# Kernel optimization log

Hardware: AMD Instinct MI355X
Metric: run time of the kernel (lower is better)

## Reference

```python
import math
import jax, jax.numpy as jnp
import numpy as np

B, T, D = 4, 4096, 1024
H = 16            # n_heads
HD = D // H       # head_dim = 64
CAP = int(4096 * 0.125)  # mod capacity k = 512
DFF = int(D * 4 * 2 / 3)  # 2730, per SwiGLU
EPS = 1e-6


def rmsnorm(x, g):
    return x * jax.lax.rsqrt(jnp.mean(x * x, axis=-1, keepdims=True) + EPS) * g


def setup_inputs() -> dict:
    key = jax.random.key(0)
    ks = jax.random.split(key, 9)
    s = lambda k, shape: (jax.random.normal(k, shape, jnp.float32) * 0.02)
    return {
        "x": jax.random.normal(ks[0], (B, T, D), jnp.float32),
        "w_router": s(ks[1], (D,)),          # router Linear(d_model,1,bias=False)
        "W_qkv": s(ks[2], (3 * D, D)),       # torch Linear weight layout [out,in]
        "W_out": s(ks[3], (D, D)),
        "g1": jnp.ones((D,), jnp.float32),   # RMSNorm weights
        "g2": jnp.ones((D,), jnp.float32),
        "W1": s(ks[4], (DFF, D)),
        "W2": s(ks[5], (DFF, D)),
        "W3": s(ks[6], (D, DFF)),
    }


def reference(x, w_router, W_qkv, W_out, g1, g2, W1, W2, W3):
    Bq, Tq, Dq = x.shape
    # --- MoD routing: top-k tokens per sequence (T > capacity) ---
    scores = x @ w_router                         # [B, T]
    _, idx = jax.lax.top_k(scores, CAP)           # [B, k], descending-score order (matches torch.topk)
    x_sel = jnp.take_along_axis(x, idx[:, :, None], axis=1)  # [B, k, D]

    # --- causal attention on the gathered subset ---
    h = rmsnorm(x_sel, g1)
    qkv = (h @ W_qkv.T).reshape(Bq, CAP, 3, H, HD)
    q, k, v = jnp.moveaxis(qkv, 2, 0)             # each [B, k, H, HD]
    att = jnp.einsum('bqhd,bkhd->bhqk', q, k) / math.sqrt(HD)
    mask = jnp.triu(jnp.ones((CAP, CAP), bool), 1)  # causal mask in gathered order
    att = jnp.where(mask, -jnp.inf, att)
    att = jax.nn.softmax(att, axis=-1)
    o = jnp.einsum('bhqk,bkhd->bqhd', att, v).reshape(Bq, CAP, Dq)
    x_attn = o @ W_out.T

    # --- SwiGLU FFN ---
    h2 = rmsnorm(x_sel + x_attn, g2)
    x_ff = (jax.nn.silu(h2 @ W1.T) * (h2 @ W2.T)) @ W3.T

    # --- combine and scatter back into the full sequence ---
    x_proc = x_sel + x_attn + x_ff                # [B, k, D]
    out = x.at[jnp.arange(Bq)[:, None], idx].set(x_proc)
    return out
```

## Files before the change

kernel.cpp:

```cpp
#include <hip/hip_runtime.h>
#include <hip/hip_bf16.h>


#define B_   4
#define T_   4096
#define D_   1024
#define H_   16
#define HD_  64
#define CAP_ 512
#define DFF_ 2730
#define DFFP 2752
#define DFFR 2816
#define M_   (B_*CAP_)

typedef __attribute__((ext_vector_type(8))) short          s16x8;
typedef __attribute__((ext_vector_type(8))) unsigned short u16x8;
typedef __attribute__((ext_vector_type(4))) float          f32x4;

__device__ __forceinline__ float bf2f(unsigned short u) {
    union { float f; unsigned int i; } v; v.i = ((unsigned int)u) << 16; return v.f;
}
__device__ __forceinline__ unsigned short f2bf(float f) {
    union { float f; unsigned int i; } v; v.f = f;
    unsigned int r = v.i + 0x7fffu + ((v.i >> 16) & 1u);
    return (unsigned short)(r >> 16);
}

__device__ __forceinline__ void gload_lds16(const unsigned short* g, unsigned short* l) {
    __builtin_amdgcn_global_load_lds(
        (const __attribute__((address_space(1))) unsigned int*)g,
        (__attribute__((address_space(3))) unsigned int*)l, 16, 0, 0);
}

__global__ __launch_bounds__(256) void k_copy_router(const float* __restrict__ x,
                                                     const float* __restrict__ wr,
                                                     float* __restrict__ out,
                                                     float* __restrict__ sc) {
    int gw   = (blockIdx.x * 256 + threadIdx.x) >> 6;
    int lane = threadIdx.x & 63;
    const float* row = x + (size_t)gw * D_;
    float* orow = out + (size_t)gw * D_;
    float s = 0.f;
#pragma unroll
    for (int p = 0; p < 4; ++p) {
        int c = p * 256 + lane * 4;
        float4 xv = *(const float4*)(row + c);
        float4 wv = *(const float4*)(wr + c);
        *(float4*)(orow + c) = xv;
        s += xv.x * wv.x + xv.y * wv.y + xv.z * wv.z + xv.w * wv.w;
    }
#pragma unroll
    for (int o = 32; o; o >>= 1) s += __shfl_xor(s, o);
    if (lane == 0) sc[gw] = s;
}

__global__ __launch_bounds__(256) void k_f2b(const float4* __restrict__ s,
                                             ushort4* __restrict__ d, int n4) {
    int i = blockIdx.x * 256 + threadIdx.x;
    int st = gridDim.x * 256;
    for (; i < n4; i += st) {
        float4 v = s[i];
        ushort4 o;
        o.x = f2bf(v.x); o.y = f2bf(v.y); o.z = f2bf(v.z); o.w = f2bf(v.w);
        d[i] = o;
    }
}

__global__ __launch_bounds__(256) void k_f2b_rowpad(const float* __restrict__ src,
                                                    unsigned short* __restrict__ dst,
                                                    int kc, int rows, int total) {
    int g = blockIdx.x * 256 + threadIdx.x;
    int st = gridDim.x * 256;
    for (; g < total; g += st) {
        int row = g / kc;
        u16x8 v = {0, 0, 0, 0, 0, 0, 0, 0};
        if (row < rows) {
            const float* s = src + ((size_t)g) * 8;
#pragma unroll
            for (int j = 0; j < 2; ++j) {
                float4 f = *(const float4*)(s + 4 * j);
                v[4*j]   = f2bf(f.x); v[4*j+1] = f2bf(f.y);
                v[4*j+2] = f2bf(f.z); v[4*j+3] = f2bf(f.w);
            }
        }
        *(u16x8*)(dst + (size_t)g * 8) = v;
    }
}

__global__ __launch_bounds__(256) void k_f2b_pad(const float* __restrict__ src,
                                                 unsigned short* __restrict__ dst,
                                                 int K, int Kp, int rows) {
    int g = blockIdx.x * 256 + threadIdx.x;
    int ng = rows * (Kp >> 3);
    int st = gridDim.x * 256;
    for (; g < ng; g += st) {
        int row = g / (Kp >> 3);
        int c = (g - row * (Kp >> 3)) << 3;
        const float* s = src + (size_t)row * K + c;
        u16x8 v;
        if (c + 8 <= K) {
#pragma unroll
            for (int j = 0; j < 4; ++j) {
                float2 f = *(const float2*)(s + 2 * j);
                v[2*j] = f2bf(f.x); v[2*j+1] = f2bf(f.y);
            }
        } else {
#pragma unroll
            for (int j = 0; j < 8; ++j) v[j] = (c + j < K) ? f2bf(s[j]) : (unsigned short)0;
        }
        *(u16x8*)(dst + (size_t)row * Kp + c) = v;
    }
}

__global__ __launch_bounds__(1024) void k_topk(const float* __restrict__ sc,
                                               int* __restrict__ idx) {
    __shared__ unsigned int hist[256];
    __shared__ unsigned long long okeys[CAP_];
    __shared__ unsigned int ecand[T_];
    __shared__ unsigned int sprefix;
    __shared__ int skneed;
    __shared__ unsigned int scnt, ecnt;
    int t = threadIdx.x;
    const float* s = sc + (size_t)blockIdx.x * T_;

    unsigned int sb[4], ei[4];
#pragma unroll
    for (int j = 0; j < 4; ++j) {
        int i = j * 1024 + t;
        union { float f; unsigned int u; } v; v.f = s[i];
        unsigned int k = (v.u & 0x80000000u) ? ~v.u : (v.u | 0x80000000u);
        sb[j] = ~k;
        ei[j] = (unsigned int)i;
    }
    if (t == 0) { sprefix = 0; skneed = CAP_; scnt = 0; ecnt = 0; }

#pragma unroll
    for (int rs = 24; rs >= 0; rs -= 8) {
        if (t < 256) hist[t] = 0;
        __syncthreads();
        unsigned int pfx = sprefix;
#pragma unroll
        for (int j = 0; j < 4; ++j) {
            if (((unsigned long long)(sb[j] ^ pfx) >> (rs + 8)) == 0ULL)
                atomicAdd(&hist[(sb[j] >> rs) & 255u], 1u);
        }
        __syncthreads();
        if (t < 64) {
            unsigned int h0 = hist[t * 4], h1 = hist[t * 4 + 1];
            unsigned int h2 = hist[t * 4 + 2], h3 = hist[t * 4 + 3];
            unsigned int lsum = h0 + h1 + h2 + h3;
            unsigned int run = lsum;
#pragma unroll
            for (int d = 1; d < 64; d <<= 1) {
                unsigned int v = __shfl_up(run, d);
                if (t >= d) run += v;
            }
            unsigned int excl = run - lsum;
            int need = skneed;
            if (excl < (unsigned int)need && run >= (unsigned int)need) {
                unsigned int cum = excl;
                int b = t * 4;
                if (cum + h0 < (unsigned int)need) { cum += h0; ++b;
                    if (cum + h1 < (unsigned int)need) { cum += h1; ++b;
                        if (cum + h2 < (unsigned int)need) { cum += h2; ++b; } } }
                sprefix = pfx | ((unsigned int)b << rs);
                skneed = need - (int)cum;
            }
        }
        __syncthreads();
    }

    unsigned int Sstar = sprefix;
    int neq = skneed;
#pragma unroll
    for (int j = 0; j < 4; ++j) {
        if (sb[j] < Sstar) {
            unsigned int p = atomicAdd(&scnt, 1u);
            okeys[p] = ((unsigned long long)sb[j] << 32) | ei[j];
        } else if (sb[j] == Sstar) {
            unsigned int p = atomicAdd(&ecnt, 1u);
            ecand[p] = ei[j];
        }
    }
    __syncthreads();
    if (t == 0) {
        unsigned int base = scnt;
        unsigned int ne = ecnt;
        for (int q = 0; q < neq; ++q) {
            unsigned int mn = 0xffffffffu; int mi = 0;
            for (unsigned int e = 0; e < ne; ++e)
                if (ecand[e] < mn) { mn = ecand[e]; mi = (int)e; }
            okeys[base + q] = ((unsigned long long)Sstar << 32) | mn;
            ecand[mi] = 0xffffffffu;
        }
    }
    __syncthreads();
    if (t < CAP_) {
        unsigned long long mine = okeys[t];
        int r = 0;
#pragma unroll 8
        for (int q = 0; q < CAP_; ++q) r += (okeys[q] < mine) ? 1 : 0;
        idx[blockIdx.x * CAP_ + r] = (int)(mine & 0xffffffffu);
    }
}

__global__ __launch_bounds__(256) void k_gather_rms(const float* __restrict__ x,
                                                    const int* __restrict__ idx,
                                                    const float* __restrict__ g,
                                                    unsigned short* __restrict__ h) {
    int r = blockIdx.x;
    int b = r >> 9;
    int src = idx[r] & (T_ - 1);
    const float* xr = x + ((size_t)b * T_ + src) * D_;
    int c = threadIdx.x * 4;
    float4 xv = *(const float4*)(xr + c);
    float ss = xv.x*xv.x + xv.y*xv.y + xv.z*xv.z + xv.w*xv.w;
#pragma unroll
    for (int o = 32; o; o >>= 1) ss += __shfl_xor(ss, o);
    __shared__ float red[4];
    int lane = threadIdx.x & 63, w = threadIdx.x >> 6;
    if (lane == 0) red[w] = ss;
    __syncthreads();
    float tot = red[0] + red[1] + red[2] + red[3];
    float scale = rsqrtf(tot * (1.f / D_) + 1e-6f);
    float4 gv = *(const float4*)(g + c);
    ushort4 hv;
    hv.x = f2bf(xv.x * scale * gv.x);
    hv.y = f2bf(xv.y * scale * gv.y);
    hv.z = f2bf(xv.z * scale * gv.z);
    hv.w = f2bf(xv.w * scale * gv.w);
    *(ushort4*)(h + (size_t)r * D_ + c) = hv;
}

__global__ __launch_bounds__(512) void k_gemm64g(const unsigned short* __restrict__ A,
                                                 const unsigned short* __restrict__ Bw,
                                                 unsigned short* __restrict__ C,
                                                 int Nout, int Kr) {
    __shared__ __align__(16) unsigned short As[2][64 * 64];
    __shared__ __align__(16) unsigned short Bs[2][128 * 64];
    int m0 = blockIdx.x * 64;
    int n0 = blockIdx.y * 128;
    int t = threadIdx.x;
    int w = t >> 6, lane = t & 63;
    int lr = lane & 15, lg = lane >> 4;
    int l8 = lane >> 3, lm8 = lane & 7;

    int arow = w * 8 + l8;
    int acb  = lm8 ^ (arow & 7);
    int brow = w * 16 + l8;
    int bcb0 = lm8 ^ (brow & 7), bcb1 = lm8 ^ ((brow + 8) & 7);

    f32x4 acc[4];
#pragma unroll
    for (int mi = 0; mi < 4; ++mi) acc[mi] = {0.f, 0.f, 0.f, 0.f};

#define STAGE_G(buf, k0)                                                          \
    {                                                                             \
        gload_lds16(A + (size_t)(m0 + arow) * Kr + (k0) + acb * 8,                \
                    &As[buf][(w * 8) * 64]);                                      \
        gload_lds16(Bw + (size_t)(n0 + brow) * Kr + (k0) + bcb0 * 8,              \
                    &Bs[buf][(w * 16) * 64]);                                     \
        gload_lds16(Bw + (size_t)(n0 + brow + 8) * Kr + (k0) + bcb1 * 8,          \
                    &Bs[buf][(w * 16 + 8) * 64]);                                 \
    }

    int nk = Kr >> 6;
    STAGE_G(0, 0);
    __syncthreads();
    for (int kt = 0; kt < nk; ++kt) {
        int cur = kt & 1;
        if (kt + 1 < nk) STAGE_G(cur ^ 1, (kt + 1) << 6);
#pragma unroll
        for (int kh = 0; kh < 2; ++kh) {
            s16x8 af[4], bf;
#pragma unroll
            for (int i = 0; i < 4; ++i) {
                int row = i * 16 + lr;
                int pb = (kh * 4 + lg) ^ (row & 7);
                af[i] = *(const s16x8*)&As[cur][row * 64 + pb * 8];
            }
            {
                int row = w * 16 + lr;
                int pb = (kh * 4 + lg) ^ (row & 7);
                bf = *(const s16x8*)&Bs[cur][row * 64 + pb * 8];
            }
#pragma unroll
            for (int mi = 0; mi < 4; ++mi)
                acc[mi] = __builtin_amdgcn_mfma_f32_16x16x32_bf16(af[mi], bf, acc[mi], 0, 0, 0);
        }
        __syncthreads();
    }
#undef STAGE_G
    int orow0 = m0 + (lg << 2);
    int col = n0 + w * 16 + lr;
    if (col < Nout) {
#pragma unroll
        for (int mi = 0; mi < 4; ++mi)
#pragma unroll
            for (int i = 0; i < 4; ++i)
                C[(size_t)(orow0 + mi * 16 + i) * Nout + col] = f2bf(acc[mi][i]);
    }
}

__global__ __launch_bounds__(512) void k_gemm64g2(const unsigned short* __restrict__ A,
                                                  const unsigned short* __restrict__ B1,
                                                  const unsigned short* __restrict__ B2,
                                                  unsigned short* __restrict__ F,
                                                  int Nout, int Kr) {
    __shared__ __align__(16) unsigned short As[2][64 * 64];
    __shared__ __align__(16) unsigned short B1s[2][128 * 64];
    __shared__ __align__(16) unsigned short B2s[2][128 * 64];
    int m0 = blockIdx.x * 64;
    int n0 = blockIdx.y * 128;
    int t = threadIdx.x;
    int w = t >> 6, lane = t & 63;
    int lr = lane & 15, lg = lane >> 4;
    int l8 = lane >> 3, lm8 = lane & 7;

    int arow = w * 8 + l8;
    int acb  = lm8 ^ (arow & 7);
    int brow = w * 16 + l8;
    int bcb0 = lm8 ^ (brow & 7), bcb1 = lm8 ^ ((brow + 8) & 7);

    f32x4 accU[4], accG[4];
#pragma unroll
    for (int mi = 0; mi < 4; ++mi) {
        accU[mi] = {0.f, 0.f, 0.f, 0.f};
        accG[mi] = {0.f, 0.f, 0.f, 0.f};
    }

#define STAGE_G2(buf, k0)                                                          \
    {                                                                              \
        gload_lds16(A + (size_t)(m0 + arow) * Kr + (k0) + acb * 8,                 \
                    &As[buf][(w * 8) * 64]);                                       \
        size_t go0 = (size_t)(n0 + brow) * Kr + (k0) + bcb0 * 8;                   \
        size_t go1 = (size_t)(n0 + brow + 8) * Kr + (k0) + bcb1 * 8;               \
        gload_lds16(B1 + go0, &B1s[buf][(w * 16) * 64]);                           \
        gload_lds16(B1 + go1, &B1s[buf][(w * 16 + 8) * 64]);                       \
        gload_lds16(B2 + go0, &B2s[buf][(w * 16) * 64]);                           \
        gload_lds16(B2 + go1, &B2s[buf][(w * 16 + 8) * 64]);                       \
    }

    int nk = Kr >> 6;
    STAGE_G2(0, 0);
    __syncthreads();
    for (int kt = 0; kt < nk; ++kt) {
        int cur = kt & 1;
        if (kt + 1 < nk) STAGE_G2(cur ^ 1, (kt + 1) << 6);
#pragma unroll
        for (int kh = 0; kh < 2; ++kh) {
            s16x8 af[4], b1f, b2f;
#pragma unroll
            for (int i = 0; i < 4; ++i) {
                int row = i * 16 + lr;
                int pb = (kh * 4 + lg) ^ (row & 7);
                af[i] = *(const s16x8*)&As[cur][row * 64 + pb * 8];
            }
            {
                int row = w * 16 + lr;
                int pb = (kh * 4 + lg) ^ (row & 7);
                b1f = *(const s16x8*)&B1s[cur][row * 64 + pb * 8];
                b2f = *(const s16x8*)&B2s[cur][row * 64 + pb * 8];
            }
#pragma unroll
            for (int mi = 0; mi < 4; ++mi) {
                accU[mi] = __builtin_amdgcn_mfma_f32_16x16x32_bf16(af[mi], b1f, accU[mi], 0, 0, 0);
                accG[mi] = __builtin_amdgcn_mfma_f32_16x16x32_bf16(af[mi], b2f, accG[mi], 0, 0, 0);
            }
        }
        __syncthreads();
    }
#undef STAGE_G2
    int orow0 = m0 + (lg << 2);
    int col = n0 + w * 16 + lr;
    if (col < Nout) {
#pragma unroll
        for (int mi = 0; mi < 4; ++mi)
#pragma unroll
            for (int i = 0; i < 4; ++i) {
                float u = accU[mi][i];
                float sl = u / (1.f + __expf(-u));
                F[(size_t)(orow0 + mi * 16 + i) * Nout + col] = f2bf(sl * accG[mi][i]);
            }
    }
}

__global__ __launch_bounds__(256) void k_attn_mfma(const unsigned short* __restrict__ qkv,
                                                   unsigned short* __restrict__ o) {
    __shared__ __align__(16) unsigned short Ks[64][72];
    __shared__ __align__(16) unsigned short Vt[64][72];
    __shared__ __align__(16) unsigned short Ps[4][16][72];
    int qt = blockIdx.x, h = blockIdx.y, b = blockIdx.z;
    int q0 = qt * 64;
    int t = threadIdx.x, w = t >> 6, lane = t & 63;
    int lr = lane & 15, lg = lane >> 4;
    const unsigned short* base = qkv + (size_t)b * CAP_ * 3 * D_;

    int qrow = q0 + w * 16 + lr;
    const unsigned short* qp = base + (size_t)qrow * 3 * D_ + h * 64;
    s16x8 aq0 = *(const s16x8*)(qp + lg * 8);
    s16x8 aq1 = *(const s16x8*)(qp + 32 + lg * 8);

    f32x4 zero = {0.f, 0.f, 0.f, 0.f};
    f32x4 oacc[4] = {zero, zero, zero, zero};
    float m_[4], l_[4];
#pragma unroll
    for (int i = 0; i < 4; ++i) { m_[i] = -3.0e38f; l_[i] = 0.f; }

    int qbase = q0 + w * 16 + lg * 4;
    int ntile = qt + 1;

    int skv = t >> 2, sc = (t & 3) * 16;
    for (int kt = 0; kt < ntile; ++kt) {
        int kv0 = kt << 6;
        {
            const unsigned short* kr = base + (size_t)(kv0 + skv) * 3 * D_ + D_     + h * 64 + sc;
            const unsigned short* vr = base + (size_t)(kv0 + skv) * 3 * D_ + 2 * D_ + h * 64 + sc;
            *(u16x8*)&Ks[skv][sc]     = *(const u16x8*)kr;
            *(u16x8*)&Ks[skv][sc + 8] = *(const u16x8*)(kr + 8);
            u16x8 v0 = *(const u16x8*)vr;
            u16x8 v1 = *(const u16x8*)(vr + 8);
#pragma unroll
            for (int j = 0; j < 8; ++j) {
                Vt[sc + j][skv]     = v0[j];
                Vt[sc + 8 + j][skv] = v1[j];
            }
        }
        __syncthreads();
        f32x4 s_[4] = {zero, zero, zero, zero};
#pragma unroll
        for (int qi = 0; qi < 4; ++qi) {
            s16x8 k0 = *(const s16x8*)&Ks[qi * 16 + lr][lg * 8];
            s16x8 k1 = *(const s16x8*)&Ks[qi * 16 + lr][32 + lg * 8];
            s_[qi] = __builtin_amdgcn_mfma_f32_16x16x32_bf16(aq0, k0, s_[qi], 0, 0, 0);
            s_[qi] = __builtin_amdgcn_mfma_f32_16x16x32_bf16(aq1, k1, s_[qi], 0, 0, 0);
        }
#pragma unroll
        for (int qi = 0; qi < 4; ++qi)
#pragma unroll
            for (int i = 0; i < 4; ++i) {
                float v = s_[qi][i] * 0.125f;
                if (kv0 + qi * 16 + lr > qbase + i) v = -3.0e38f;
                s_[qi][i] = v;
            }
        float pm[4];
#pragma unroll
        for (int i = 0; i < 4; ++i)
            pm[i] = fmaxf(fmaxf(s_[0][i], s_[1][i]), fmaxf(s_[2][i], s_[3][i]));
#pragma unroll
        for (int d = 1; d < 16; d <<= 1) {
#pragma unroll
            for (int i = 0; i < 4; ++i) pm[i] = fmaxf(pm[i], __shfl_xor(pm[i], d));
        }
        float p[4][4], ps[4], scl[4];
#pragma unroll
        for (int i = 0; i < 4; ++i) {
            float mn = fmaxf(m_[i], pm[i]);
            scl[i] = __expf(m_[i] - mn);
            ps[i] = 0.f;
#pragma unroll
            for (int qi = 0; qi < 4; ++qi) {
                p[qi][i] = __expf(s_[qi][i] - mn);
                ps[i] += p[qi][i];
            }
            m_[i] = mn;
        }
#pragma unroll
        for (int d = 1; d < 16; d <<= 1) {
#pragma unroll
            for (int i = 0; i < 4; ++i) ps[i] += __shfl_xor(ps[i], d);
        }
#pragma unroll
        for (int i = 0; i < 4; ++i) l_[i] = l_[i] * scl[i] + ps[i];
#pragma unroll
        for (int dg = 0; dg < 4; ++dg)
#pragma unroll
            for (int i = 0; i < 4; ++i) oacc[dg][i] *= scl[i];
#pragma unroll
        for (int qi = 0; qi < 4; ++qi)
#pragma unroll
            for (int i = 0; i < 4; ++i)
                Ps[w][lg * 4 + i][qi * 16 + lr] = f2bf(p[qi][i]);
        __syncthreads();
        s16x8 pa0 = *(const s16x8*)&Ps[w][lr][lg * 8];
        s16x8 pa1 = *(const s16x8*)&Ps[w][lr][32 + lg * 8];
#pragma unroll
        for (int dg = 0; dg < 4; ++dg) {
            s16x8 vf0 = *(const s16x8*)&Vt[dg * 16 + lr][lg * 8];
            s16x8 vf1 = *(const s16x8*)&Vt[dg * 16 + lr][32 + lg * 8];
            oacc[dg] = __builtin_amdgcn_mfma_f32_16x16x32_bf16(pa0, vf0, oacc[dg], 0, 0, 0);
            oacc[dg] = __builtin_amdgcn_mfma_f32_16x16x32_bf16(pa1, vf1, oacc[dg], 0, 0, 0);
        }
        __syncthreads();
    }
    unsigned short* orow = o + ((size_t)(b * CAP_ + qbase)) * D_ + h * 64;
#pragma unroll
    for (int i = 0; i < 4; ++i) {
        float inv = 1.f / l_[i];
#pragma unroll
        for (int dg = 0; dg < 4; ++dg)
            orow[(size_t)i * D_ + dg * 16 + lr] = f2bf(oacc[dg][i] * inv);
    }
}

__global__ __launch_bounds__(256) void k_add_rms(const float* __restrict__ x,
                                                 const int* __restrict__ idx,
                                                 const unsigned short* __restrict__ xattn,
                                                 const float* __restrict__ g,
                                                 unsigned short* __restrict__ y,
                                                 unsigned short* __restrict__ h) {
    int r = blockIdx.x;
    int b = r >> 9;
    int src = idx[r] & (T_ - 1);
    int c = threadIdx.x * 4;
    const float* xr = x + ((size_t)b * T_ + src) * D_;
    float4 xv = *(const float4*)(xr + c);
    size_t off = (size_t)r * D_ + c;
    ushort4 a4 = *(const ushort4*)(xattn + off);
    float v0 = xv.x + bf2f(a4.x);
    float v1 = xv.y + bf2f(a4.y);
    float v2 = xv.z + bf2f(a4.z);
    float v3 = xv.w + bf2f(a4.w);
    float ss = v0*v0 + v1*v1 + v2*v2 + v3*v3;
#pragma unroll
    for (int o = 32; o; o >>= 1) ss += __shfl_xor(ss, o);
    __shared__ float red[4];
    int lane = threadIdx.x & 63, w = threadIdx.x >> 6;
    if (lane == 0) red[w] = ss;
    __syncthreads();
    float tot = red[0] + red[1] + red[2] + red[3];
    float scale = rsqrtf(tot * (1.f / D_) + 1e-6f);
    ushort4 yv;
    yv.x = f2bf(v0); yv.y = f2bf(v1); yv.z = f2bf(v2); yv.w = f2bf(v3);
    *(ushort4*)(y + off) = yv;
    float4 gv = *(const float4*)(g + c);
    ushort4 hv;
    hv.x = f2bf(v0 * scale * gv.x);
    hv.y = f2bf(v1 * scale * gv.y);
    hv.z = f2bf(v2 * scale * gv.z);
    hv.w = f2bf(v3 * scale * gv.w);
    *(ushort4*)(h + off) = hv;
}

__global__ __launch_bounds__(256) void k_scatter(const unsigned short* __restrict__ y,
                                                 const unsigned short* __restrict__ xff,
                                                 const int* __restrict__ idx,
                                                 float* __restrict__ out) {
    int r = blockIdx.x;
    int b = r >> 9;
    int dst = idx[r] & (T_ - 1);
    int c = threadIdx.x * 4;
    size_t src = (size_t)r * D_ + c;
    ushort4 a4 = *(const ushort4*)(y + src);
    ushort4 f4 = *(const ushort4*)(xff + src);
    float4 o4;
    o4.x = bf2f(a4.x) + bf2f(f4.x);
    o4.y = bf2f(a4.y) + bf2f(f4.y);
    o4.z = bf2f(a4.z) + bf2f(f4.z);
    o4.w = bf2f(a4.w) + bf2f(f4.w);
    *(float4*)(out + ((size_t)b * T_ + dst) * D_ + c) = o4;
}

extern "C" void kernel_launch(void* const* d_in, const int* in_sizes, int n_in,
                              void* d_out, int out_size, void* d_ws, size_t ws_size,
                              hipStream_t stream) {
    const float* x     = (const float*)d_in[0];
    const float* w_rt  = (const float*)d_in[1];
    const float* W_qkv = (const float*)d_in[2];
    const float* W_out = (const float*)d_in[3];
    const float* g1    = (const float*)d_in[4];
    const float* g2    = (const float*)d_in[5];
    const float* W1    = (const float*)d_in[6];
    const float* W2    = (const float*)d_in[7];
    const float* W3    = (const float*)d_in[8];
    float* out = (float*)d_out;

    char* p = (char*)d_ws;
    float* scores = (float*)p;
    int*   idx    = (int*)(p + 65536);
    size_t off = 131072;
    const size_t WPAD = (size_t)DFFR * D_;
    unsigned short* WBIG = (unsigned short*)(p + off); off += 2 * WPAD * 2;
    unsigned short* WB2  = WBIG + WPAD;
    unsigned short* R1   = (unsigned short*)(p + off); off += (size_t)M_*3*D_*2;
    unsigned short* R2   = (unsigned short*)(p + off); off += (size_t)M_*D_*2;
    unsigned short* R3   = (unsigned short*)(p + off); off += (size_t)M_*D_*2;
    unsigned short* R4   = (unsigned short*)(p + off); off += (size_t)M_*D_*2;

    unsigned short* h1    = R2;
    unsigned short* qkvb  = R1;
    unsigned short* attno = R2;
    unsigned short* xattn = R3;
    unsigned short* ybuf  = R4;
    unsigned short* h2b   = R2;
    unsigned short* fbuf  = R1;
    unsigned short* xffb  = R3;

    k_copy_router<<<(B_*T_) / 4, 256, 0, stream>>>(x, w_rt, out, scores);
    k_topk<<<B_, 1024, 0, stream>>>(scores, idx);
    k_gather_rms<<<M_, 256, 0, stream>>>(x, idx, g1, h1);
    k_f2b<<<2048, 256, 0, stream>>>((const float4*)W_qkv, (ushort4*)WBIG, (3*D_*D_) / 4);
    k_gemm64g<<<dim3(M_/64, 3*D_/128), 512, 0, stream>>>(h1, WBIG, qkvb, 3*D_, D_);
    k_attn_mfma<<<dim3(CAP_/64, H_, B_), 256, 0, stream>>>(qkvb, attno);
    k_f2b<<<1024, 256, 0, stream>>>((const float4*)W_out, (ushort4*)WBIG, (D_*D_) / 4);
    k_gemm64g<<<dim3(M_/64, D_/128), 512, 0, stream>>>(attno, WBIG, xattn, D_, D_);
    k_add_rms<<<M_, 256, 0, stream>>>(x, idx, xattn, g2, ybuf, h2b);
    k_f2b_rowpad<<<2048, 256, 0, stream>>>(W1, WBIG, D_/8, DFF_, DFFR*(D_/8));
    k_f2b_rowpad<<<2048, 256, 0, stream>>>(W2, WB2,  D_/8, DFF_, DFFR*(D_/8));
    k_gemm64g2<<<dim3(M_/64, DFFR/128), 512, 0, stream>>>(h2b, WBIG, WB2, fbuf,
                                                          DFFP, D_);
    k_f2b_pad<<<2048, 256, 0, stream>>>(W3, WBIG, DFF_, DFFP, D_);
    k_gemm64g<<<dim3(M_/64, D_/128), 512, 0, stream>>>(fbuf, WBIG, xffb, D_, DFFP);
    k_scatter<<<M_, 256, 0, stream>>>(ybuf, xffb, idx, out);
}
```

Measured before the change: 200.4 us.

## Fuse scatter into FFN GEMM epilogue, merge W1/W2 casts, 128x128 QKV GEMM

The final down-projection GEMM now adds the residual and scatters fp32 results straight into the output, which removes the separate scatter kernel and the bf16 round-trip of x_ff. The W1 and W2 fp32-to-bf16 conversions are merged into one launch. The QKV projection switches to a new 128x128-tile GEMM that gives each wave more data reuse. The fused epilogue writes scalar, column-strided values with an index lookup per element, which may coalesce worse than the old vectorised scatter.

```diff
diff --git a/kernel.cpp b/kernel.cpp
--- a/kernel.cpp
+++ b/kernel.cpp
@@ -66,24 +66,31 @@
     }
 }
 
-__global__ __launch_bounds__(256) void k_f2b_rowpad(const float* __restrict__ src,
-                                                    unsigned short* __restrict__ dst,
-                                                    int kc, int rows, int total) {
+__global__ __launch_bounds__(256) void k_f2b_rowpad2(const float* __restrict__ s1,
+                                                     const float* __restrict__ s2,
+                                                     unsigned short* __restrict__ d1,
+                                                     unsigned short* __restrict__ d2,
+                                                     int kc, int rows, int total) {
     int g = blockIdx.x * 256 + threadIdx.x;
     int st = gridDim.x * 256;
     for (; g < total; g += st) {
         int row = g / kc;
-        u16x8 v = {0, 0, 0, 0, 0, 0, 0, 0};
+        u16x8 v1 = {0,0,0,0,0,0,0,0}, v2 = {0,0,0,0,0,0,0,0};
         if (row < rows) {
-            const float* s = src + ((size_t)g) * 8;
+            const float* p1 = s1 + ((size_t)g) * 8;
+            const float* p2 = s2 + ((size_t)g) * 8;
 #pragma unroll
             for (int j = 0; j < 2; ++j) {
-                float4 f = *(const float4*)(s + 4 * j);
-                v[4*j]   = f2bf(f.x); v[4*j+1] = f2bf(f.y);
-                v[4*j+2] = f2bf(f.z); v[4*j+3] = f2bf(f.w);
-            }
-        }
-        *(u16x8*)(dst + (size_t)g * 8) = v;
+                float4 f1 = *(const float4*)(p1 + 4 * j);
+                float4 f2 = *(const float4*)(p2 + 4 * j);
+                v1[4*j] = f2bf(f1.x); v1[4*j+1] = f2bf(f1.y);
+                v1[4*j+2] = f2bf(f1.z); v1[4*j+3] = f2bf(f1.w);
+                v2[4*j] = f2bf(f2.x); v2[4*j+1] = f2bf(f2.y);
+                v2[4*j+2] = f2bf(f2.z); v2[4*j+3] = f2bf(f2.w);
+            }
+        }
+        *(u16x8*)(d1 + (size_t)g * 8) = v1;
+        *(u16x8*)(d2 + (size_t)g * 8) = v2;
     }
 }
 
@@ -232,10 +239,95 @@
     *(ushort4*)(h + (size_t)r * D_ + c) = hv;
 }
 
+__global__ __launch_bounds__(512) void k_gemm128g(const unsigned short* __restrict__ A,
+                                                  const unsigned short* __restrict__ Bw,
+                                                  unsigned short* __restrict__ C,
+                                                  int Nout, int Kr) {
+    __shared__ __align__(16) unsigned short As[2][128 * 64];
+    __shared__ __align__(16) unsigned short Bs[2][128 * 64];
+    int m0 = blockIdx.x * 128;
+    int n0 = blockIdx.y * 128;
+    int t = threadIdx.x;
+    int w = t >> 6, lane = t & 63;
+    int lr = lane & 15, lg = lane >> 4;
+    int l8 = lane >> 3, lm8 = lane & 7;
+    int wm = (w >> 2) * 64, wn = (w & 3) * 32;
+
+    int srow = w * 16 + l8;
+    int cb0 = lm8 ^ (srow & 7), cb1 = lm8 ^ ((srow + 8) & 7);
+
+    f32x4 acc[4][2];
+#pragma unroll
+    for (int mi = 0; mi < 4; ++mi)
+#pragma unroll
+        for (int ni = 0; ni < 2; ++ni) acc[mi][ni] = {0.f, 0.f, 0.f, 0.f};
+
+#define STAGE_128(buf, k0)                                                        \
+    {                                                                             \
+        gload_lds16(A + (size_t)(m0 + srow) * Kr + (k0) + cb0 * 8,                \
+                    &As[buf][(w * 16) * 64]);                                     \
+        gload_lds16(A + (size_t)(m0 + srow + 8) * Kr + (k0) + cb1 * 8,            \
+                    &As[buf][(w * 16 + 8) * 64]);                                 \
+        gload_lds16(Bw + (size_t)(n0 + srow) * Kr + (k0) + cb0 * 8,               \
+                    &Bs[buf][(w * 16) * 64]);                                     \
+        gload_lds16(Bw + (size_t)(n0 + srow + 8) * Kr + (k0) + cb1 * 8,           \
+                    &Bs[buf][(w * 16 + 8) * 64]);                                 \
+    }
+
+    int nk = Kr >> 6;
+    STAGE_128(0, 0);
+    __syncthreads();
+    for (int kt = 0; kt < nk; ++kt) {
+        int cur = kt & 1;
+        if (kt + 1 < nk) STAGE_128(cur ^ 1, (kt + 1) << 6);
+#pragma unroll
+        for (int kh = 0; kh < 2; ++kh) {
+            s16x8 af[4], bf[2];
+#pragma unroll
+            for (int i = 0; i < 4; ++i) {
+                int row = wm + i * 16 + lr;
+                int pb = (kh * 4 + lg) ^ (row & 7);
+                af[i] = *(const s16x8*)&As[cur][row * 64 + pb * 8];
+            }
+#pragma unroll
+            for (int i = 0; i < 2; ++i) {
+                int row = wn + i * 16 + lr;
+                int pb = (kh * 4 + lg) ^ (row & 7);
+                bf[i] = *(const s16x8*)&Bs[cur][row * 64 + pb * 8];
+            }
+#pragma unroll
+            for (int mi = 0; mi < 4; ++mi)
+#pragma unroll
+                for (int ni = 0; ni < 2; ++ni)
+                    acc[mi][ni] = __builtin_amdgcn_mfma_f32_16x16x32_bf16(af[mi], bf[ni],
+                                                                          acc[mi][ni], 0, 0, 0);
+        }
+        __syncthreads();
+    }
+#undef STAGE_128
+    int orow0 = m0 + wm + (lg << 2);
+    int ocol0 = n0 + wn + lr;
+#pragma unroll
+    for (int ni = 0; ni < 2; ++ni) {
+        int col = ocol0 + ni * 16;
+        if (col < Nout) {
+#pragma unroll
+            for (int mi = 0; mi < 4; ++mi)
+#pragma unroll
+                for (int i = 0; i < 4; ++i)
+                    C[(size_t)(orow0 + mi * 16 + i) * Nout + col] = f2bf(acc[mi][ni][i]);
+        }
+    }
+}
+
+template<int EPI>
 __global__ __launch_bounds__(512) void k_gemm64g(const unsigned short* __restrict__ A,
                                                  const unsigned short* __restrict__ Bw,
                                                  unsigned short* __restrict__ C,
-                                                 int Nout, int Kr) {
+                                                 int Nout, int Kr,
+                                                 const unsigned short* __restrict__ Y,
+                                                 const int* __restrict__ idxp,
+                                                 float* __restrict__ outp) {
     __shared__ __align__(16) unsigned short As[2][64 * 64];
     __shared__ __align__(16) unsigned short Bs[2][128 * 64];
     int m0 = blockIdx.x * 64;
@@ -297,8 +389,17 @@
 #pragma unroll
         for (int mi = 0; mi < 4; ++mi)
 #pragma unroll
-            for (int i = 0; i < 4; ++i)
-                C[(size_t)(orow0 + mi * 16 + i) * Nout + col] = f2bf(acc[mi][i]);
+            for (int i = 0; i < 4; ++i) {
+                int r = orow0 + mi * 16 + i;
+                if (EPI == 2) {
+                    int b = r >> 9;
+                    int dst = idxp[r] & (T_ - 1);
+                    float yv = bf2f(Y[(size_t)r * D_ + col]);
+                    outp[((size_t)(b * T_ + dst)) * D_ + col] = yv + acc[mi][i];
+                } else {
+                    C[(size_t)r * Nout + col] = f2bf(acc[mi][i]);
+                }
+            }
     }
 }
 
@@ -542,25 +643,6 @@
     *(ushort4*)(h + off) = hv;
 }
 
-__global__ __launch_bounds__(256) void k_scatter(const unsigned short* __restrict__ y,
-                                                 const unsigned short* __restrict__ xff,
-                                                 const int* __restrict__ idx,
-                                                 float* __restrict__ out) {
-    int r = blockIdx.x;
-    int b = r >> 9;
-    int dst = idx[r] & (T_ - 1);
-    int c = threadIdx.x * 4;
-    size_t src = (size_t)r * D_ + c;
-    ushort4 a4 = *(const ushort4*)(y + src);
-    ushort4 f4 = *(const ushort4*)(xff + src);
-    float4 o4;
-    o4.x = bf2f(a4.x) + bf2f(f4.x);
-    o4.y = bf2f(a4.y) + bf2f(f4.y);
-    o4.z = bf2f(a4.z) + bf2f(f4.z);
-    o4.w = bf2f(a4.w) + bf2f(f4.w);
-    *(float4*)(out + ((size_t)b * T_ + dst) * D_ + c) = o4;
-}
-
 extern "C" void kernel_launch(void* const* d_in, const int* in_sizes, int n_in,
                               void* d_out, int out_size, void* d_ws, size_t ws_size,
                               hipStream_t stream) {
@@ -594,22 +676,22 @@
     unsigned short* ybuf  = R4;
     unsigned short* h2b   = R2;
     unsigned short* fbuf  = R1;
-    unsigned short* xffb  = R3;
 
     k_copy_router<<<(B_*T_) / 4, 256, 0, stream>>>(x, w_rt, out, scores);
     k_topk<<<B_, 1024, 0, stream>>>(scores, idx);
     k_gather_rms<<<M_, 256, 0, stream>>>(x, idx, g1, h1);
     k_f2b<<<2048, 256, 0, stream>>>((const float4*)W_qkv, (ushort4*)WBIG, (3*D_*D_) / 4);
-    k_gemm64g<<<dim3(M_/64, 3*D_/128), 512, 0, stream>>>(h1, WBIG, qkvb, 3*D_, D_);
+    k_gemm128g<<<dim3(M_/128, 3*D_/128), 512, 0, stream>>>(h1, WBIG, qkvb, 3*D_, D_);
     k_attn_mfma<<<dim3(CAP_/64, H_, B_), 256, 0, stream>>>(qkvb, attno);
     k_f2b<<<1024, 256, 0, stream>>>((const float4*)W_out, (ushort4*)WBIG, (D_*D_) / 4);
-    k_gemm64g<<<dim3(M_/64, D_/128), 512, 0, stream>>>(attno, WBIG, xattn, D_, D_);
+    k_gemm64g<0><<<dim3(M_/64, D_/128), 512, 0, stream>>>(attno, WBIG, xattn, D_, D_,
+                                                          nullptr, nullptr, nullptr);
     k_add_rms<<<M_, 256, 0, stream>>>(x, idx, xattn, g2, ybuf, h2b);
-    k_f2b_rowpad<<<2048, 256, 0, stream>>>(W1, WBIG, D_/8, DFF_, DFFR*(D_/8));
-    k_f2b_rowpad<<<2048, 256, 0, stream>>>(W2, WB2,  D_/8, DFF_, DFFR*(D_/8));
+    k_f2b_rowpad2<<<2048, 256, 0, stream>>>(W1, W2, WBIG, WB2, D_/8, DFF_,
+                                            DFFR*(D_/8));
     k_gemm64g2<<<dim3(M_/64, DFFR/128), 512, 0, stream>>>(h2b, WBIG, WB2, fbuf,
                                                           DFFP, D_);
     k_f2b_pad<<<2048, 256, 0, stream>>>(W3, WBIG, DFF_, DFFP, D_);
-    k_gemm64g<<<dim3(M_/64, D_/128), 512, 0, stream>>>(fbuf, WBIG, xffb, D_, DFFP);
-    k_scatter<<<M_, 256, 0, stream>>>(ybuf, xffb, idx, out);
-}
+    k_gemm64g<2><<<dim3(M_/64, D_/128), 512, 0, stream>>>(fbuf, WBIG, nullptr, D_, DFFP,
+                                                          ybuf, idx, out);
+}
```

Result: faster. 195.0 us (-2.7%).
